# Kernel optimization log

Hardware: AMD Instinct MI355X
Metric: run time of the kernel (lower is better)

Reference implementation:

```python
import jax, jax.numpy as jnp
import numpy as np

# DeformConv3d hyperparams (from init_kwargs)
STRIDE = (1, 1, 1)
PAD = (1, 1, 1)
DIL = (1, 1, 1)
GROUPS = 1
DEFORM_GROUPS = 1  # reference assumes dg == 1


def setup_inputs() -> dict:
    key = jax.random.key(0)
    k1, k2, k3, k4 = jax.random.split(key, 4)
    x = jax.random.normal(k1, (2, 32, 24, 24, 24), jnp.float32)
    # offset channels = 3 * dg * kD*kH*kW = 81, layout [k_idx, (dz,dy,dx)]
    offset = jax.random.normal(k2, (2, 81, 24, 24, 24), jnp.float32)
    weight = jax.random.normal(k3, (64, 32, 3, 3, 3), jnp.float32) * 0.05
    bias = jax.random.normal(k4, (64,), jnp.float32) * 0.05
    return {"x": x, "offset": offset, "weight": weight, "bias": bias}


def _deform_conv3d(x, offset, weight, bias):
    B, C, D, H, W = x.shape
    Cout, Cg, kD, kH, kW = weight.shape
    sD, sH, sW = STRIDE
    pD, pH, pW = PAD
    dD, dH, dW = DIL
    Kn = kD * kH * kW
    Do = (D + 2 * pD - dD * (kD - 1) - 1) // sD + 1
    Ho = (H + 2 * pH - dH * (kH - 1) - 1) // sH + 1
    Wo = (W + 2 * pW - dW * (kW - 1) - 1) // sW + 1
    N = Do * Ho * Wo

    # offset: [B, Kn*3, Do,Ho,Wo] -> [B, Kn, 3, N]
    off = offset.reshape(B, Kn, 3, N)

    # kernel tap grid [Kn]
    kz, ky, kx = jnp.meshgrid(jnp.arange(kD), jnp.arange(kH), jnp.arange(kW), indexing='ij')
    kz, ky, kx = kz.reshape(Kn), ky.reshape(Kn), kx.reshape(Kn)
    # output grid [N]
    oz, oy, ox = jnp.meshgrid(jnp.arange(Do), jnp.arange(Ho), jnp.arange(Wo), indexing='ij')
    oz, oy, ox = oz.reshape(N), oy.reshape(N), ox.reshape(N)

    # sampling coords [B, Kn, N]
    z = (oz[None, None, :] * sD - pD) + kz[None, :, None] * dD + off[:, :, 0]
    y = (oy[None, None, :] * sH - pH) + ky[None, :, None] * dH + off[:, :, 1]
    xx = (ox[None, None, :] * sW - pW) + kx[None, :, None] * dW + off[:, :, 2]

    z0 = jnp.floor(z); fz = z - z0
    y0 = jnp.floor(y); fy = y - y0
    x0 = jnp.floor(xx); fx = xx - x0

    x_flat = x.reshape(B, C, D * H * W)
    acc = jnp.zeros((B, C, Kn * N), x.dtype)
    # 8 trilinear corners (fixed small loop)
    for dz in (0, 1):
        iz = z0 + dz
        wz = fz if dz else (1.0 - fz)
        for dy in (0, 1):
            iy = y0 + dy
            wy = fy if dy else (1.0 - fy)
            for dx in (0, 1):
                ix = x0 + dx
                wx = fx if dx else (1.0 - fx)
                valid = ((iz >= 0) & (iz < D) & (iy >= 0) & (iy < H)
                         & (ix >= 0) & (ix < W))
                w = (wz * wy * wx) * valid.astype(x.dtype)  # [B,Kn,N]
                izc = jnp.clip(iz, 0, D - 1).astype(jnp.int32)
                iyc = jnp.clip(iy, 0, H - 1).astype(jnp.int32)
                ixc = jnp.clip(ix, 0, W - 1).astype(jnp.int32)
                idx = (izc * H + iyc) * W + ixc  # [B,Kn,N]
                g = jnp.take_along_axis(x_flat, idx.reshape(B, 1, Kn * N), axis=2)
                acc = acc + g * w.reshape(B, 1, Kn * N)

    # im2col columns ordered (c, kz, ky, kx) to match weight layout
    cols = acc.reshape(B, C * Kn, N)
    Cpg = C // GROUPS
    Opg = Cout // GROUPS
    cols_g = cols.reshape(B, GROUPS, Cpg * Kn, N)
    w_g = weight.reshape(GROUPS, Opg, Cpg * Kn)
    out = jnp.einsum('gok,bgkn->bgon', w_g, cols_g).reshape(B, Cout, N)
    out = out + bias[None, :, None]
    return out.reshape(B, Cout, Do, Ho, Wo)


def reference(x, offset, weight, bias):
    return _deform_conv3d(x, offset, weight, bias)
```

## Files before the change

### kernel.cpp

```cpp
#include <hip/hip_runtime.h>
#include <hip/hip_fp16.h>


constexpr int B   = 2;
constexpr int C   = 32;
constexpr int D   = 24, H = 24, W = 24;
constexpr int CO  = 64;
constexpr int KN  = 27;
constexpr int DHW = D * H * W;
constexpr int N   = DHW;
constexpr int CK  = C * KN;

constexpr int TZ = 2, TY = 4, TX = 4;
constexpr int LDZ = 8, LDY = 10, LDX = 10;
constexpr int NVOX = LDZ * LDY * LDX;
constexpr int MBM  = 3;

constexpr int TPB_MAIN = 256;
constexpr int NBLK     = B * 12 * 6 * 6;

constexpr int PREPX_BLKS = (B * DHW) / 256;
constexpr int PREPW_BLKS = (CO * CK) / 256;

using h8v   = __attribute__((ext_vector_type(8))) _Float16;
using f32x4 = __attribute__((ext_vector_type(4))) float;

__device__ __forceinline__ h8v splat8(float w) {
    const _Float16 h = (_Float16)w;
    h8v r;
    #pragma unroll
    for (int i = 0; i < 8; ++i) r[i] = h;
    return r;
}

__device__ __forceinline__ unsigned pack2h(float a, float b) {
    const _Float16 ha = (_Float16)a, hb = (_Float16)b;
    unsigned short ua, ub;
    __builtin_memcpy(&ua, &ha, 2);
    __builtin_memcpy(&ub, &hb, 2);
    return (unsigned)ua | ((unsigned)ub << 16);
}

__global__ __launch_bounds__(256)
void prep_fused(const float* __restrict__ x, const float* __restrict__ wgt,
                _Float16* __restrict__ xT, _Float16* __restrict__ wp) {
    const int bid = blockIdx.x;
    if (bid < PREPX_BLKS) {
        __shared__ unsigned s_t[256 * 21];
        const int tid = threadIdx.x;
        const int v0  = bid * 256;
        const int b   = (v0 >= DHW) ? 1 : 0;
        const int vox = (v0 - b * DHW) + tid;
        const float* xb = x + (size_t)(b * C) * DHW + vox;
        #pragma unroll
        for (int c2 = 0; c2 < 16; ++c2) {
            const float f0 = xb[(size_t)(2 * c2)     * DHW];
            const float f1 = xb[(size_t)(2 * c2 + 1) * DHW];
            s_t[tid * 21 + c2] = pack2h(f0, f1);
        }
        __syncthreads();
        unsigned r[16];
        #pragma unroll
        for (int j = 0; j < 16; ++j) r[j] = s_t[tid * 21 + j];
        int4* dst = reinterpret_cast<int4*>(xT + ((size_t)(v0 + tid)) * 32);
        dst[0] = make_int4(r[0],  r[1],  r[2],  r[3]);
        dst[1] = make_int4(r[4],  r[5],  r[6],  r[7]);
        dst[2] = make_int4(r[8],  r[9],  r[10], r[11]);
        dst[3] = make_int4(r[12], r[13], r[14], r[15]);
    } else {
        const int idx   = (bid - PREPX_BLKS) * 256 + threadIdx.x;
        const int j     = idx & 7;
        const int lane  = (idx >> 3) & 63;
        const int t     = idx >> 9;
        const int otile = t / 27;
        const int kstep = t - otile * 27;
        const int o     = otile * 16 + (lane & 15);
        const int c     = 8 * (lane >> 4) + j;
        wp[idx] = (_Float16)wgt[(size_t)o * CK + c * KN + kstep];
    }
}

__device__ __forceinline__ int clamp0(int v, int hi) {
    return min(max(v, 0), hi);
}

__global__ __launch_bounds__(TPB_MAIN, 3)
void deform_main(const float* __restrict__ off,
                 const _Float16* __restrict__ xT,
                 const _Float16* __restrict__ wp,
                 const float* __restrict__ bias,
                 float* __restrict__ out) {
    __shared__ h8v s_x[NVOX * 4];

    const int tid  = threadIdx.x;
    const int lane = tid & 63;
    const int wv   = tid >> 6;
    const int pg   = wv >> 1;
    const int kh   = wv & 1;
    const int p    = lane & 15;
    const int q    = lane >> 4;

    const int bid = blockIdx.x;
    int t = (bid & 7) * 108 + (bid >> 3);
    int b = 0;
    if (t >= 432) { b = 1; t -= 432; }
    const int tz = t / 36;
    const int rt = t - tz * 36;
    const int ty = rt / 6;
    const int tx = rt - ty * 6;
    const int oz0 = tz * TZ, oy0 = ty * TY, ox0 = tx * TX;
    const int tbz = oz0 - MBM, tby = oy0 - MBM, tbx = ox0 - MBM;

    const h8v* xbase = reinterpret_cast<const h8v*>(xT) + (size_t)b * DHW * 4;

    for (int i = tid; i < NVOX * 4; i += TPB_MAIN) {
        const int v  = i >> 2;
        const int c  = i & 3;
        const int vz = v / (LDY * LDX);
        const int vr = v - vz * (LDY * LDX);
        const int vy = vr / LDX;
        const int vx = vr - vy * LDX;
        const int gz = clamp0(tbz + vz, D - 1);
        const int gy = clamp0(tby + vy, H - 1);
        const int gx = clamp0(tbx + vx, W - 1);
        const int gvox = (gz * H + gy) * W + gx;
        s_x[v * 4 + ((c + v) & 3)] = xbase[(size_t)gvox * 4 + c];
    }
    __syncthreads();

    const int pz = pg, py = p >> 2, px = p & 3;
    const int oz = oz0 + pz, oy = oy0 + py, ox = ox0 + px;
    const int n  = (oz * H + oy) * W + ox;
    const float* offp  = off + (size_t)(b * 81) * N + n;
    const h8v*   wbase = reinterpret_cast<const h8v*>(wp);

    const int k0 = kh ? 14 : 0;
    const int k1 = kh ? 27 : 14;

    f32x4 acc[4];
    #pragma unroll
    for (int ot = 0; ot < 4; ++ot) acc[ot] = (f32x4){0.f, 0.f, 0.f, 0.f};

    float offz = offp[(size_t)(k0 * 3 + 0) * N];
    float offy = offp[(size_t)(k0 * 3 + 1) * N];
    float offx = offp[(size_t)(k0 * 3 + 2) * N];

    #pragma unroll 1
    for (int ks = k0; ks < k1; ++ks) {
        const int kn = (ks + 1 < k1) ? (ks + 1) : ks;
        const float nfz = offp[(size_t)(kn * 3 + 0) * N];
        const float nfy = offp[(size_t)(kn * 3 + 1) * N];
        const float nfx = offp[(size_t)(kn * 3 + 2) * N];

        const int kz = ks / 9;
        const int kr = ks - kz * 9;
        const int ky = kr / 3;
        const int kx = kr - ky * 3;

        h8v afr[4];
        #pragma unroll
        for (int ot = 0; ot < 4; ++ot)
            afr[ot] = wbase[(ot * 27 + ks) * 64 + lane];

        const float z  = (float)(oz - 1 + kz) + offz;
        const float y  = (float)(oy - 1 + ky) + offy;
        const float xx = (float)(ox - 1 + kx) + offx;
        const float zf = floorf(z), yf = floorf(y), xf = floorf(xx);
        const float fz = z - zf, fy = y - yf, fx = xx - xf;
        const int z0 = (int)zf, y0 = (int)yf, x0 = (int)xf;

        float cw[8];
        #pragma unroll
        for (int cr = 0; cr < 8; ++cr) {
            const int cz = cr >> 2, cy = (cr >> 1) & 1, cx = cr & 1;
            const int iz = z0 + cz, iy = y0 + cy, ix = x0 + cx;
            const bool vd = ((unsigned)iz < (unsigned)D) &&
                            ((unsigned)iy < (unsigned)H) &&
                            ((unsigned)ix < (unsigned)W);
            const float wz = cz ? fz : 1.0f - fz;
            const float wy = cy ? fy : 1.0f - fy;
            const float wx = cx ? fx : 1.0f - fx;
            cw[cr] = vd ? (wz * wy * wx) : 0.0f;
        }

        const int rz = z0 - tbz, ry = y0 - tby, rx = x0 - tbx;
        const bool in = ((unsigned)rz < (unsigned)(LDZ - 1)) &&
                        ((unsigned)ry < (unsigned)(LDY - 1)) &&
                        ((unsigned)rx < (unsigned)(LDX - 1));

        h8v v8[8];
        if (in) {
            const int rv0 = (rz * LDY + ry) * LDX + rx;
            #pragma unroll
            for (int cr = 0; cr < 8; ++cr) {
                const int rv = rv0 + (cr >> 2) * (LDY * LDX)
                             + ((cr >> 1) & 1) * LDX + (cr & 1);
                v8[cr] = s_x[rv * 4 + ((q + rv) & 3)];
            }
        }
        if (!in) {
            #pragma unroll
            for (int cr = 0; cr < 8; ++cr) {
                const int cz = cr >> 2, cy = (cr >> 1) & 1, cx = cr & 1;
                const int izc = clamp0(z0 + cz, D - 1);
                const int iyc = clamp0(y0 + cy, H - 1);
                const int ixc = clamp0(x0 + cx, W - 1);
                const int gvox = (izc * H + iyc) * W + ixc;
                v8[cr] = xbase[(size_t)gvox * 4 + q];
            }
        }

        h8v bfr = splat8(0.0f);
        #pragma unroll
        for (int cr = 0; cr < 8; ++cr)
            bfr += v8[cr] * splat8(cw[cr]);

        #pragma unroll
        for (int ot = 0; ot < 4; ++ot)
            acc[ot] = __builtin_amdgcn_mfma_f32_16x16x32_f16(afr[ot], bfr,
                                                             acc[ot], 0, 0, 0);

        offz = nfz; offy = nfy; offx = nfx;
    }

    __syncthreads();
    float4* s_red = reinterpret_cast<float4*>(s_x);
    if (kh == 1) {
        float4* dst = &s_red[((size_t)pg * 64 + lane) * 4];
        #pragma unroll
        for (int ot = 0; ot < 4; ++ot)
            dst[ot] = make_float4(acc[ot][0], acc[ot][1], acc[ot][2], acc[ot][3]);
    }
    __syncthreads();
    if (kh == 0) {
        const float4* src = &s_red[((size_t)pg * 64 + lane) * 4];
        #pragma unroll
        for (int ot = 0; ot < 4; ++ot) {
            const float4 tv = src[ot];
            acc[ot][0] += tv.x; acc[ot][1] += tv.y;
            acc[ot][2] += tv.z; acc[ot][3] += tv.w;
        }
        #pragma unroll
        for (int ot = 0; ot < 4; ++ot) {
            #pragma unroll
            for (int r = 0; r < 4; ++r) {
                const int o = ot * 16 + q * 4 + r;
                out[((size_t)(b * CO + o)) * N + n] = acc[ot][r] + bias[o];
            }
        }
    }
}

extern "C" void kernel_launch(void* const* d_in, const int* in_sizes, int n_in,
                              void* d_out, int out_size, void* d_ws, size_t ws_size,
                              hipStream_t stream) {
    const float* x    = (const float*)d_in[0];
    const float* off  = (const float*)d_in[1];
    const float* wgt  = (const float*)d_in[2];
    const float* bias = (const float*)d_in[3];
    float* out = (float*)d_out;

    _Float16* xT = (_Float16*)d_ws;
    _Float16* wp = (_Float16*)((char*)d_ws + 1769472);

    prep_fused<<<PREPX_BLKS + PREPW_BLKS, 256, 0, stream>>>(x, wgt, xT, wp);
    deform_main<<<NBLK, TPB_MAIN, 0, stream>>>(off, xT, wp, bias, out);
}
```

Before: 100.7 us.

## Precompute trilinear weights and compact out-of-window samples in shared memory

Adds a block-wide pre-pass in which every (position, tap) task computes its trilinear corner weights and window index once and stores them in shared memory. Samples that fall outside the shared window are collected into a compacted list through an LDS atomic counter. These are gathered from global memory cooperatively by all threads, so the main MFMA loop no longer runs divergent per-lane global fallbacks. The cost is more LDS use, which lowers launch-bounds occupancy from 3 to 2 blocks, plus extra barriers and a second offset read for the out-of-window tasks.

```diff
diff --git a/kernel.cpp b/kernel.cpp
--- a/kernel.cpp
+++ b/kernel.cpp
@@ -15,6 +15,9 @@
 constexpr int LDZ = 8, LDY = 10, LDX = 10;
 constexpr int NVOX = LDZ * LDY * LDX;
 constexpr int MBM  = 3;
+constexpr int NPOS  = 32;
+constexpr int NTASK = NPOS * KN;
+constexpr int CAP   = 160;
 
 constexpr int TPB_MAIN = 256;
 constexpr int NBLK     = B * 12 * 6 * 6;
@@ -25,8 +28,7 @@
 using h8v   = __attribute__((ext_vector_type(8))) _Float16;
 using f32x4 = __attribute__((ext_vector_type(4))) float;
 
-__device__ __forceinline__ h8v splat8(float w) {
-    const _Float16 h = (_Float16)w;
+__device__ __forceinline__ h8v splat8h(_Float16 h) {
     h8v r;
     #pragma unroll
     for (int i = 0; i < 8; ++i) r[i] = h;
@@ -39,6 +41,10 @@
     __builtin_memcpy(&ua, &ha, 2);
     __builtin_memcpy(&ub, &hb, 2);
     return (unsigned)ua | ((unsigned)ub << 16);
+}
+
+__device__ __forceinline__ int clamp0(int v, int hi) {
+    return min(max(v, 0), hi);
 }
 
 __global__ __launch_bounds__(256)
@@ -80,17 +86,18 @@
     }
 }
 
-__device__ __forceinline__ int clamp0(int v, int hi) {
-    return min(max(v, 0), hi);
-}
-
-__global__ __launch_bounds__(TPB_MAIN, 3)
+__global__ __launch_bounds__(TPB_MAIN, 2)
 void deform_main(const float* __restrict__ off,
                  const _Float16* __restrict__ xT,
                  const _Float16* __restrict__ wp,
                  const float* __restrict__ bias,
                  float* __restrict__ out) {
-    __shared__ h8v s_x[NVOX * 4];
+    __shared__ h8v      s_win[NVOX * 4];
+    __shared__ h8v      s_cw [NTASK];
+    __shared__ unsigned s_meta[NTASK];
+    __shared__ h8v      s_mval[CAP * 4];
+    __shared__ unsigned short s_mlist[CAP];
+    __shared__ int      s_cnt;
 
     const int tid  = threadIdx.x;
     const int lane = tid & 63;
@@ -101,17 +108,22 @@
     const int q    = lane >> 4;
 
     const int bid = blockIdx.x;
-    int t = (bid & 7) * 108 + (bid >> 3);
+    int t0 = (bid & 7) * 108 + (bid >> 3);
     int b = 0;
-    if (t >= 432) { b = 1; t -= 432; }
-    const int tz = t / 36;
-    const int rt = t - tz * 36;
+    if (t0 >= 432) { b = 1; t0 -= 432; }
+    const int tz = t0 / 36;
+    const int rt = t0 - tz * 36;
     const int ty = rt / 6;
     const int tx = rt - ty * 6;
     const int oz0 = tz * TZ, oy0 = ty * TY, ox0 = tx * TX;
     const int tbz = oz0 - MBM, tby = oy0 - MBM, tbx = ox0 - MBM;
 
-    const h8v* xbase = reinterpret_cast<const h8v*>(xT) + (size_t)b * DHW * 4;
+    const h8v*   xbase = reinterpret_cast<const h8v*>(xT) + (size_t)b * DHW * 4;
+    const float* offb  = off + (size_t)(b * 81) * N;
+    const h8v*   wbase = reinterpret_cast<const h8v*>(wp);
+
+    if (tid == 0) s_cnt = 0;
+    __syncthreads();
 
     for (int i = tid; i < NVOX * 4; i += TPB_MAIN) {
         const int v  = i >> 2;
@@ -124,43 +136,23 @@
         const int gy = clamp0(tby + vy, H - 1);
         const int gx = clamp0(tbx + vx, W - 1);
         const int gvox = (gz * H + gy) * W + gx;
-        s_x[v * 4 + ((c + v) & 3)] = xbase[(size_t)gvox * 4 + c];
-    }
-    __syncthreads();
-
-    const int pz = pg, py = p >> 2, px = p & 3;
-    const int oz = oz0 + pz, oy = oy0 + py, ox = ox0 + px;
-    const int n  = (oz * H + oy) * W + ox;
-    const float* offp  = off + (size_t)(b * 81) * N + n;
-    const h8v*   wbase = reinterpret_cast<const h8v*>(wp);
-
-    const int k0 = kh ? 14 : 0;
-    const int k1 = kh ? 27 : 14;
-
-    f32x4 acc[4];
-    #pragma unroll
-    for (int ot = 0; ot < 4; ++ot) acc[ot] = (f32x4){0.f, 0.f, 0.f, 0.f};
-
-    float offz = offp[(size_t)(k0 * 3 + 0) * N];
-    float offy = offp[(size_t)(k0 * 3 + 1) * N];
-    float offx = offp[(size_t)(k0 * 3 + 2) * N];
-
-    #pragma unroll 1
-    for (int ks = k0; ks < k1; ++ks) {
-        const int kn = (ks + 1 < k1) ? (ks + 1) : ks;
-        const float nfz = offp[(size_t)(kn * 3 + 0) * N];
-        const float nfy = offp[(size_t)(kn * 3 + 1) * N];
-        const float nfx = offp[(size_t)(kn * 3 + 2) * N];
-
+        s_win[v * 4 + ((c + v) & 3)] = xbase[(size_t)gvox * 4 + c];
+    }
+
+    for (int t = tid; t < NTASK; t += TPB_MAIN) {
+        const int tp = t & 31;
+        const int ks = t >> 5;
+        const int pz = tp >> 4, py = (tp >> 2) & 3, px = tp & 3;
+        const int oz = oz0 + pz, oy = oy0 + py, ox = ox0 + px;
+        const int n  = (oz * H + oy) * W + ox;
         const int kz = ks / 9;
         const int kr = ks - kz * 9;
         const int ky = kr / 3;
         const int kx = kr - ky * 3;
 
-        h8v afr[4];
-        #pragma unroll
-        for (int ot = 0; ot < 4; ++ot)
-            afr[ot] = wbase[(ot * 27 + ks) * 64 + lane];
+        const float offz = offb[(size_t)(ks * 3 + 0) * N + n];
+        const float offy = offb[(size_t)(ks * 3 + 1) * N + n];
+        const float offx = offb[(size_t)(ks * 3 + 2) * N + n];
 
         const float z  = (float)(oz - 1 + kz) + offz;
         const float y  = (float)(oy - 1 + ky) + offy;
@@ -169,7 +161,7 @@
         const float fz = z - zf, fy = y - yf, fx = xx - xf;
         const int z0 = (int)zf, y0 = (int)yf, x0 = (int)xf;
 
-        float cw[8];
+        h8v cw8;
         #pragma unroll
         for (int cr = 0; cr < 8; ++cr) {
             const int cz = cr >> 2, cy = (cr >> 1) & 1, cx = cr & 1;
@@ -180,25 +172,118 @@
             const float wz = cz ? fz : 1.0f - fz;
             const float wy = cy ? fy : 1.0f - fy;
             const float wx = cx ? fx : 1.0f - fx;
-            cw[cr] = vd ? (wz * wy * wx) : 0.0f;
+            cw8[cr] = (_Float16)(vd ? (wz * wy * wx) : 0.0f);
         }
 
         const int rz = z0 - tbz, ry = y0 - tby, rx = x0 - tbx;
-        const bool in = ((unsigned)rz < (unsigned)(LDZ - 1)) &&
-                        ((unsigned)ry < (unsigned)(LDY - 1)) &&
-                        ((unsigned)rx < (unsigned)(LDX - 1));
+        const bool in = ((unsigned)rz <= (unsigned)(LDZ - 2)) &&
+                        ((unsigned)ry <= (unsigned)(LDY - 2)) &&
+                        ((unsigned)rx <= (unsigned)(LDX - 2));
+        const int rzc = clamp0(rz, LDZ - 2);
+        const int ryc = clamp0(ry, LDY - 2);
+        const int rxc = clamp0(rx, LDX - 2);
+        const int rv0 = (rzc * LDY + ryc) * LDX + rxc;
+
+        unsigned mslot = 0xFFu;
+        if (!in) {
+            const int sl = atomicAdd(&s_cnt, 1);
+            if (sl < CAP) { mslot = (unsigned)sl; s_mlist[sl] = (unsigned short)t; }
+            else          { mslot = 0xFEu; }
+        }
+        s_cw[t]   = cw8;
+        s_meta[t] = (unsigned)rv0 | (mslot << 16);
+    }
+    __syncthreads();
+
+    const int cnt = min(s_cnt, CAP);
+    for (int i = tid; i < cnt * 4; i += TPB_MAIN) {
+        const int s  = i >> 2;
+        const int q2 = i & 3;
+        const int t  = s_mlist[s];
+        const int tp = t & 31;
+        const int ks = t >> 5;
+        const int pz = tp >> 4, py = (tp >> 2) & 3, px = tp & 3;
+        const int oz = oz0 + pz, oy = oy0 + py, ox = ox0 + px;
+        const int n  = (oz * H + oy) * W + ox;
+        const int kz = ks / 9;
+        const int kr = ks - kz * 9;
+        const int ky = kr / 3;
+        const int kx = kr - ky * 3;
+
+        const float offz = offb[(size_t)(ks * 3 + 0) * N + n];
+        const float offy = offb[(size_t)(ks * 3 + 1) * N + n];
+        const float offx = offb[(size_t)(ks * 3 + 2) * N + n];
+        const int z0 = (int)floorf((float)(oz - 1 + kz) + offz);
+        const int y0 = (int)floorf((float)(oy - 1 + ky) + offy);
+        const int x0 = (int)floorf((float)(ox - 1 + kx) + offx);
+
+        const h8v cw8 = s_cw[t];
+        h8v acc = splat8h((_Float16)0.0f);
+        #pragma unroll
+        for (int cr = 0; cr < 8; ++cr) {
+            const int cz = cr >> 2, cy = (cr >> 1) & 1, cx = cr & 1;
+            const int izc = clamp0(z0 + cz, D - 1);
+            const int iyc = clamp0(y0 + cy, H - 1);
+            const int ixc = clamp0(x0 + cx, W - 1);
+            const int gvox = (izc * H + iyc) * W + ixc;
+            acc += xbase[(size_t)gvox * 4 + q2] * splat8h(cw8[cr]);
+        }
+        s_mval[s * 4 + q2] = acc;
+    }
+    __syncthreads();
+
+    const int phat = pg * 16 + p;
+    const int pz = phat >> 4, py = (phat >> 2) & 3, px = phat & 3;
+    const int oz = oz0 + pz, oy = oy0 + py, ox = ox0 + px;
+    const int n  = (oz * H + oy) * W + ox;
+
+    const int k0 = kh ? 14 : 0;
+    const int k1 = kh ? 27 : 14;
+
+    f32x4 acc[4];
+    #pragma unroll
+    for (int ot = 0; ot < 4; ++ot) acc[ot] = (f32x4){0.f, 0.f, 0.f, 0.f};
+
+    #pragma unroll 1
+    for (int ks = k0; ks < k1; ++ks) {
+        h8v afr[4];
+        #pragma unroll
+        for (int ot = 0; ot < 4; ++ot)
+            afr[ot] = wbase[(ot * 27 + ks) * 64 + lane];
+
+        const int t = ks * 32 + phat;
+        const h8v      cw8  = s_cw[t];
+        const unsigned meta = s_meta[t];
+        const int      rv0  = (int)(meta & 1023u);
+        const unsigned ms   = (meta >> 16) & 0xFFu;
 
         h8v v8[8];
-        if (in) {
-            const int rv0 = (rz * LDY + ry) * LDX + rx;
-            #pragma unroll
-            for (int cr = 0; cr < 8; ++cr) {
-                const int rv = rv0 + (cr >> 2) * (LDY * LDX)
-                             + ((cr >> 1) & 1) * LDX + (cr & 1);
-                v8[cr] = s_x[rv * 4 + ((q + rv) & 3)];
-            }
-        }
-        if (!in) {
+        #pragma unroll
+        for (int cr = 0; cr < 8; ++cr) {
+            const int rv = rv0 + (cr >> 2) * (LDY * LDX)
+                         + ((cr >> 1) & 1) * LDX + (cr & 1);
+            v8[cr] = s_win[rv * 4 + ((q + rv) & 3)];
+        }
+        h8v bfr = splat8h((_Float16)0.0f);
+        #pragma unroll
+        for (int cr = 0; cr < 8; ++cr)
+            bfr += v8[cr] * splat8h(cw8[cr]);
+
+        if (ms < 0xFEu)
+            bfr = s_mval[(int)ms * 4 + q];
+
+        if (ms == 0xFEu) {
+            const int kz = ks / 9;
+            const int kr = ks - kz * 9;
+            const int ky = kr / 3;
+            const int kx = kr - ky * 3;
+            const float offz = offb[(size_t)(ks * 3 + 0) * N + n];
+            const float offy = offb[(size_t)(ks * 3 + 1) * N + n];
+            const float offx = offb[(size_t)(ks * 3 + 2) * N + n];
+            const int z0 = (int)floorf((float)(oz - 1 + kz) + offz);
+            const int y0 = (int)floorf((float)(oy - 1 + ky) + offy);
+            const int x0 = (int)floorf((float)(ox - 1 + kx) + offx);
+            h8v a2 = splat8h((_Float16)0.0f);
             #pragma unroll
             for (int cr = 0; cr < 8; ++cr) {
                 const int cz = cr >> 2, cy = (cr >> 1) & 1, cx = cr & 1;
@@ -206,25 +291,19 @@
                 const int iyc = clamp0(y0 + cy, H - 1);
                 const int ixc = clamp0(x0 + cx, W - 1);
                 const int gvox = (izc * H + iyc) * W + ixc;
-                v8[cr] = xbase[(size_t)gvox * 4 + q];
+                a2 += xbase[(size_t)gvox * 4 + q] * splat8h(cw8[cr]);
             }
-        }
-
-        h8v bfr = splat8(0.0f);
-        #pragma unroll
-        for (int cr = 0; cr < 8; ++cr)
-            bfr += v8[cr] * splat8(cw[cr]);
+            bfr = a2;
+        }
 
         #pragma unroll
         for (int ot = 0; ot < 4; ++ot)
             acc[ot] = __builtin_amdgcn_mfma_f32_16x16x32_f16(afr[ot], bfr,
                                                              acc[ot], 0, 0, 0);
-
-        offz = nfz; offy = nfy; offx = nfx;
-    }
-
-    __syncthreads();
-    float4* s_red = reinterpret_cast<float4*>(s_x);
+    }
+
+    __syncthreads();
+    float4* s_red = reinterpret_cast<float4*>(s_cw);
     if (kh == 1) {
         float4* dst = &s_red[((size_t)pg * 64 + lane) * 4];
         #pragma unroll
```

After: 100.2 us. About the same (-0.6%).
